# Kernel optimization log

Measured on AMD Instinct MI355X. Metric: run time of the kernel, lower is better.

Reference implementation:

```python
import jax, jax.numpy as jnp
import numpy as np

N = 8192
IN_F = 512
OUT_F = 256
ALPHA = 0.2


def setup_inputs() -> dict:
    key = jax.random.key(0)
    k1, k2, k3 = jax.random.split(key, 3)
    inp = jax.random.normal(k1, (N, IN_F), dtype=jnp.float32)
    # xavier_uniform with gain=1.414
    def xavier(k, shape, gain=1.414):
        fan_in, fan_out = shape[0], shape[1]
        bound = gain * np.sqrt(6.0 / (fan_in + fan_out))
        return jax.random.uniform(k, shape, jnp.float32, -bound, bound)
    W = xavier(k2, (IN_F, OUT_F))
    a = xavier(k3, (2 * OUT_F, 1))
    adj = jnp.ones((N, N), dtype=jnp.int32)  # unused by the original forward
    return {"input": inp, "adj": adj, "W": W, "a": a}


def reference(input, adj, W, a):
    # h: [N, F]
    h = input @ W
    F_ = h.shape[1]
    # Original builds [N, N, 2F] pairwise concat then matmul with a [2F,1].
    # Equivalent: e[i,j] = leaky_relu(h[i] . a[:F] + h[j] . a[F:])
    src = h @ a[:F_, 0]   # [N]
    dst = h @ a[F_:, 0]   # [N]
    e = jax.nn.leaky_relu(src[:, None] + dst[None, :], negative_slope=ALPHA)  # [N, N]
    attention = jax.nn.softmax(e, axis=1)  # adj is NOT applied in original code
    h_prime = attention @ h  # [N, F]
    return jax.nn.elu(h_prime)
```

## Files before the change

### kernel.cpp

```cpp
#include <hip/hip_runtime.h>
#include <math.h>

#define NR 8192
#define INF_ 512
#define OUTF 256
#define ALPHA 0.2f

__global__ __launch_bounds__(256) void k_gemm(const float* __restrict__ A,
                                              const float* __restrict__ W,
                                              float* __restrict__ H) {
    __shared__ float As[16][68];
    __shared__ float Bs[16][68];
    const int tid = threadIdx.x;
    const int brow = blockIdx.x * 64;
    const int bcol = blockIdx.y * 64;
    const int tx = tid & 15, ty = tid >> 4;
    const int ar = tid >> 2;
    const int ac = (tid & 3) << 2;
    const int br = tid >> 4;
    const int bc = (tid & 15) << 2;

    float acc[4][4] = {};
    for (int k0 = 0; k0 < INF_; k0 += 16) {
        float4 av = *(const float4*)(A + (size_t)(brow + ar) * INF_ + k0 + ac);
        float4 bv = *(const float4*)(W + (size_t)(k0 + br) * OUTF + bcol + bc);
        __syncthreads();
        As[ac + 0][ar] = av.x; As[ac + 1][ar] = av.y;
        As[ac + 2][ar] = av.z; As[ac + 3][ar] = av.w;
        *(float4*)&Bs[br][bc] = bv;
        __syncthreads();
#pragma unroll
        for (int kk = 0; kk < 16; ++kk) {
            float4 a4 = *(const float4*)&As[kk][ty * 4];
            float4 b4 = *(const float4*)&Bs[kk][tx * 4];
            acc[0][0] = fmaf(a4.x, b4.x, acc[0][0]); acc[0][1] = fmaf(a4.x, b4.y, acc[0][1]);
            acc[0][2] = fmaf(a4.x, b4.z, acc[0][2]); acc[0][3] = fmaf(a4.x, b4.w, acc[0][3]);
            acc[1][0] = fmaf(a4.y, b4.x, acc[1][0]); acc[1][1] = fmaf(a4.y, b4.y, acc[1][1]);
            acc[1][2] = fmaf(a4.y, b4.z, acc[1][2]); acc[1][3] = fmaf(a4.y, b4.w, acc[1][3]);
            acc[2][0] = fmaf(a4.z, b4.x, acc[2][0]); acc[2][1] = fmaf(a4.z, b4.y, acc[2][1]);
            acc[2][2] = fmaf(a4.z, b4.z, acc[2][2]); acc[2][3] = fmaf(a4.z, b4.w, acc[2][3]);
            acc[3][0] = fmaf(a4.w, b4.x, acc[3][0]); acc[3][1] = fmaf(a4.w, b4.y, acc[3][1]);
            acc[3][2] = fmaf(a4.w, b4.z, acc[3][2]); acc[3][3] = fmaf(a4.w, b4.w, acc[3][3]);
        }
    }
#pragma unroll
    for (int m = 0; m < 4; ++m) {
        float4 o = make_float4(acc[m][0], acc[m][1], acc[m][2], acc[m][3]);
        *(float4*)(H + (size_t)(brow + ty * 4 + m) * OUTF + bcol + tx * 4) = o;
    }
}

__global__ __launch_bounds__(256) void k_srcdst(const float* __restrict__ H,
                                                const float* __restrict__ a,
                                                float* __restrict__ src,
                                                float* __restrict__ dst) {
    const int wv = threadIdx.x >> 6;
    const int ln = threadIdx.x & 63;
    const int row = blockIdx.x * 4 + wv;
    float4 hv = *(const float4*)(H + (size_t)row * OUTF + ln * 4);
    float4 a1 = *(const float4*)(a + ln * 4);
    float4 a2 = *(const float4*)(a + OUTF + ln * 4);
    float s = hv.x * a1.x + hv.y * a1.y + hv.z * a1.z + hv.w * a1.w;
    float d = hv.x * a2.x + hv.y * a2.y + hv.z * a2.z + hv.w * a2.w;
#pragma unroll
    for (int o = 32; o > 0; o >>= 1) {
        s += __shfl_down(s, o);
        d += __shfl_down(d, o);
    }
    if (ln == 0) { src[row] = s; dst[row] = d; }
}

__global__ __launch_bounds__(256) void k_rank(const float* __restrict__ dstv,
                                              float* __restrict__ dsts,
                                              int* __restrict__ perm) {
    __shared__ float key[NR];
    const int tid = threadIdx.x;
#pragma unroll
    for (int i = 0; i < 8; ++i)
        *(float4*)(key + 4 * (tid + 256 * i)) = *(const float4*)(dstv + 4 * (tid + 256 * i));
    __syncthreads();
    const int el = blockIdx.x * 32 + (tid >> 3);
    const int sub = tid & 7;
    const float my = key[el];
    const int sbase = sub << 10;
    int cnt = 0;
#pragma unroll 4
    for (int i = 0; i < 256; ++i) {
        const int off = ((i + sub) << 2) & 1023;
        const int k0 = sbase + off;
        float4 v = *(const float4*)(key + k0);
        cnt += (int)((v.x < my) | ((v.x == my) & (k0 + 0 < el)));
        cnt += (int)((v.y < my) | ((v.y == my) & (k0 + 1 < el)));
        cnt += (int)((v.z < my) | ((v.z == my) & (k0 + 2 < el)));
        cnt += (int)((v.w < my) | ((v.w == my) & (k0 + 3 < el)));
    }
    cnt += __shfl_down(cnt, 4);
    cnt += __shfl_down(cnt, 2);
    cnt += __shfl_down(cnt, 1);
    if (sub == 0) {
        dsts[cnt] = my;
        perm[cnt] = el;
    }
}

__global__ __launch_bounds__(1024) void k_scan(const float* __restrict__ dsts,
                                               float* __restrict__ wplus,
                                               float* __restrict__ wminus,
                                               float* __restrict__ Splus,
                                               float* __restrict__ Sminus) {
    __shared__ float wsP[16], wsM[16];
    const int t = threadIdx.x;
    const int lane = t & 63;
    const float D = dsts[NR - 1];
    float4 v0 = *(const float4*)(dsts + t * 8);
    float4 v1 = *(const float4*)(dsts + t * 8 + 4);
    float vv[8] = {v0.x, v0.y, v0.z, v0.w, v1.x, v1.y, v1.z, v1.w};
    float wp[8], wm[8];
    float sp = 0.f, sm = 0.f;
#pragma unroll
    for (int j = 0; j < 8; ++j) {
        wp[j] = expf(vv[j] - D);
        wm[j] = expf(ALPHA * vv[j]);
        sp += wp[j]; sm += wm[j];
    }
    *(float4*)(wplus + t * 8)      = make_float4(wp[0], wp[1], wp[2], wp[3]);
    *(float4*)(wplus + t * 8 + 4)  = make_float4(wp[4], wp[5], wp[6], wp[7]);
    *(float4*)(wminus + t * 8)     = make_float4(wm[0], wm[1], wm[2], wm[3]);
    *(float4*)(wminus + t * 8 + 4) = make_float4(wm[4], wm[5], wm[6], wm[7]);
    float ip = sp, im = sm;
#pragma unroll
    for (int o = 1; o < 64; o <<= 1) {
        float tp = __shfl_up(ip, o);
        float tm = __shfl_up(im, o);
        if (lane >= o) { ip += tp; im += tm; }
    }
    if (lane == 63) { wsP[t >> 6] = ip; wsM[t >> 6] = im; }
    __syncthreads();
    if (t < 16) {
        float a = wsP[t], b = wsM[t];
#pragma unroll
        for (int o = 1; o < 16; o <<= 1) {
            float ta = __shfl_up(a, o);
            float tb = __shfl_up(b, o);
            if (t >= o) { a += ta; b += tb; }
        }
        wsP[t] = a; wsM[t] = b;
    }
    __syncthreads();
    const int w = t >> 6;
    float rp = (w ? wsP[w - 1] : 0.f) + (ip - sp);
    float rm = (w ? wsM[w - 1] : 0.f) + (im - sm);
#pragma unroll
    for (int j = 0; j < 8; ++j) {
        rp += wp[j]; rm += wm[j];
        Splus[t * 8 + j + 1] = rp;
        Sminus[t * 8 + j + 1] = rm;
    }
    if (t == 0) { Splus[0] = 0.f; Sminus[0] = 0.f; }
}

__global__ __launch_bounds__(256) void k_chunksum(const float* __restrict__ H,
                                                  const int* __restrict__ perm,
                                                  const float* __restrict__ wplus,
                                                  const float* __restrict__ wminus,
                                                  float* __restrict__ chunkP,
                                                  float* __restrict__ chunkM) {
    const int b = blockIdx.x, f = threadIdx.x;
    float aP = 0.f, aM = 0.f;
#pragma unroll 4
    for (int k = 0; k < 32; ++k) {
        int g = b * 32 + k;
        int p = perm[g];
        float hv = H[(size_t)p * OUTF + f];
        aP = fmaf(wplus[g], hv, aP);
        aM = fmaf(wminus[g], hv, aM);
    }
    chunkP[b * OUTF + f] = aP;
    chunkM[b * OUTF + f] = aM;
}

__global__ __launch_bounds__(64) void k_chunkscan(const float* __restrict__ chunkP,
                                                  const float* __restrict__ chunkM,
                                                  float* __restrict__ offP,
                                                  float* __restrict__ offM,
                                                  float* __restrict__ PrefP,
                                                  float* __restrict__ PrefM) {
    const int f = blockIdx.x;
    const bool minus = (blockIdx.y != 0);
    const float* sv = minus ? chunkM : chunkP;
    float* dv = minus ? offM : offP;
    float* tot = minus ? PrefM : PrefP;
    const int l = threadIdx.x;
    float v0 = sv[(4 * l + 0) * OUTF + f];
    float v1 = sv[(4 * l + 1) * OUTF + f];
    float v2 = sv[(4 * l + 2) * OUTF + f];
    float v3 = sv[(4 * l + 3) * OUTF + f];
    float s = v0 + v1 + v2 + v3;
    float incl = s;
#pragma unroll
    for (int o = 1; o < 64; o <<= 1) {
        float t = __shfl_up(incl, o);
        if (l >= o) incl += t;
    }
    float excl = incl - s;
    dv[(4 * l + 0) * OUTF + f] = excl;
    dv[(4 * l + 1) * OUTF + f] = excl + v0;
    dv[(4 * l + 2) * OUTF + f] = excl + v0 + v1;
    dv[(4 * l + 3) * OUTF + f] = excl + v0 + v1 + v2;
    if (l == 63) tot[(size_t)NR * OUTF + f] = incl;
}

__global__ __launch_bounds__(256) void k_writepref(const float* __restrict__ H,
                                                   const int* __restrict__ perm,
                                                   const float* __restrict__ wplus,
                                                   const float* __restrict__ wminus,
                                                   const float* __restrict__ offP,
                                                   const float* __restrict__ offM,
                                                   float* __restrict__ PrefP,
                                                   float* __restrict__ PrefM) {
    const int b = blockIdx.x, f = threadIdx.x;
    float aP = offP[b * OUTF + f];
    float aM = offM[b * OUTF + f];
    for (int k = 0; k < 32; ++k) {
        int g = b * 32 + k;
        PrefP[(size_t)g * OUTF + f] = aP;
        PrefM[(size_t)g * OUTF + f] = aM;
        int p = perm[g];
        float hv = H[(size_t)p * OUTF + f];
        aP = fmaf(wplus[g], hv, aP);
        aM = fmaf(wminus[g], hv, aM);
    }
}

__global__ __launch_bounds__(256) void k_out(const float* __restrict__ src,
                                             const float* __restrict__ dsts,
                                             const float* __restrict__ Splus,
                                             const float* __restrict__ Sminus,
                                             const float* __restrict__ PrefP,
                                             const float* __restrict__ PrefM,
                                             float* __restrict__ out) {
    const int i = blockIdx.x, f = threadIdx.x;
    const float si = src[i];
    const float D = dsts[NR - 1];
    const float thr = -si;
    int lo = 0, hi = NR;
    while (lo < hi) {
        int mid = (lo + hi) >> 1;
        if (dsts[mid] <= thr) lo = mid + 1; else hi = mid;
    }
    const int t = lo;
    const float cP = expf(si + D);
    const float cM = expf(ALPHA * si);
    const float SP = Splus[NR] - Splus[t];
    const float SM = Sminus[t];
    const float inv = 1.f / (cP * SP + cM * SM);
    const float pP = PrefP[(size_t)NR * OUTF + f] - PrefP[(size_t)t * OUTF + f];
    const float pM = PrefM[(size_t)t * OUTF + f];
    const float v = (cP * pP + cM * pM) * inv;
    out[(size_t)i * OUTF + f] = v > 0.f ? v : expm1f(v);
}

extern "C" void kernel_launch(void* const* d_in, const int* in_sizes, int n_in,
                              void* d_out, int out_size, void* d_ws, size_t ws_size,
                              hipStream_t stream) {
    const float* X = (const float*)d_in[0];
    const float* W = (const float*)d_in[2];
    const float* a = (const float*)d_in[3];
    float* out = (float*)d_out;

    char* ws = (char*)d_ws;
    size_t off = 0;
    auto carve = [&](size_t bytes) -> void* {
        void* p = ws + off;
        off += (bytes + 1023) & ~(size_t)1023;
        return p;
    };
    float* H      = (float*)carve((size_t)NR * OUTF * 4);
    float* src    = (float*)carve(NR * 4);
    float* dstv   = (float*)carve(NR * 4);
    float* dsts   = (float*)carve(NR * 4);
    int*   perm   = (int*)carve(NR * 4);
    float* wplus  = (float*)carve(NR * 4);
    float* wminus = (float*)carve(NR * 4);
    float* Splus  = (float*)carve((NR + 1) * 4);
    float* Sminus = (float*)carve((NR + 1) * 4);
    float* chunkP = (float*)carve(256 * OUTF * 4);
    float* chunkM = (float*)carve(256 * OUTF * 4);
    float* offP   = (float*)carve(256 * OUTF * 4);
    float* offM   = (float*)carve(256 * OUTF * 4);
    float* PrefP  = (float*)carve((size_t)(NR + 1) * OUTF * 4);
    float* PrefM  = (float*)carve((size_t)(NR + 1) * OUTF * 4);

    k_gemm<<<dim3(NR / 64, OUTF / 64), 256, 0, stream>>>(X, W, H);
    k_srcdst<<<NR / 4, 256, 0, stream>>>(H, a, src, dstv);
    k_rank<<<NR / 32, 256, 0, stream>>>(dstv, dsts, perm);
    k_scan<<<1, 1024, 0, stream>>>(dsts, wplus, wminus, Splus, Sminus);
    k_chunksum<<<256, 256, 0, stream>>>(H, perm, wplus, wminus, chunkP, chunkM);
    k_chunkscan<<<dim3(OUTF, 2), 64, 0, stream>>>(chunkP, chunkM, offP, offM, PrefP, PrefM);
    k_writepref<<<256, 256, 0, stream>>>(H, perm, wplus, wminus, offP, offM, PrefP, PrefM);
    k_out<<<NR, 256, 0, stream>>>(src, dsts, Splus, Sminus, PrefP, PrefM, out);
}
```

Measured before the change: 444.4 us.

## Use split-bf16 MFMA GEMM and fuse post-GEMM stages into one cooperative kernel

Replaces the FP32 SIMT GEMM with a matrix-core GEMM that splits each operand into hi and lo bf16 parts and uses three MFMAs per tile to keep near-FP32 accuracy. The seven post-GEMM kernels (src/dst, rank sort, scan, chunk sums, chunk scan, prefix write, output) are merged into one 256-block cooperative kernel separated by grid syncs. The scan is parallelised across blocks, and the output stage handles 32 rows per block. This removes launch overhead and uses the matrix cores, at the cost of grid-sync latency, lower parallelism in the final stage, and some precision loss from the bf16 split.

```diff
diff --git a/kernel.cpp b/kernel.cpp
--- a/kernel.cpp
+++ b/kernel.cpp
@@ -1,263 +1,296 @@
 #include <hip/hip_runtime.h>
+#include <hip/hip_cooperative_groups.h>
 #include <math.h>
+
+namespace cg = cooperative_groups;
 
 #define NR 8192
 #define INF_ 512
 #define OUTF 256
 #define ALPHA 0.2f
 
-__global__ __launch_bounds__(256) void k_gemm(const float* __restrict__ A,
+typedef __attribute__((ext_vector_type(8))) short bf16x8;
+typedef __attribute__((ext_vector_type(4))) float f32x4;
+
+#define MFMA(a, b, c) __builtin_amdgcn_mfma_f32_16x16x32_bf16((a), (b), (c), 0, 0, 0)
+
+__device__ __forceinline__ ushort f2bf(float x) {
+    unsigned u = __float_as_uint(x);
+    return (ushort)((u + 0x7fff + ((u >> 16) & 1)) >> 16);
+}
+__device__ __forceinline__ float bf2f(ushort b) { return __uint_as_float((unsigned)b << 16); }
+
+__global__ __launch_bounds__(256) void k_gemm(const float* __restrict__ X,
                                               const float* __restrict__ W,
                                               float* __restrict__ H) {
-    __shared__ float As[16][68];
-    __shared__ float Bs[16][68];
+    __shared__ ushort sAhi[2048], sAlo[2048], sBhi[2048], sBlo[2048];
     const int tid = threadIdx.x;
-    const int brow = blockIdx.x * 64;
-    const int bcol = blockIdx.y * 64;
-    const int tx = tid & 15, ty = tid >> 4;
-    const int ar = tid >> 2;
-    const int ac = (tid & 3) << 2;
-    const int br = tid >> 4;
-    const int bc = (tid & 15) << 2;
-
-    float acc[4][4] = {};
-    for (int k0 = 0; k0 < INF_; k0 += 16) {
-        float4 av = *(const float4*)(A + (size_t)(brow + ar) * INF_ + k0 + ac);
-        float4 bv = *(const float4*)(W + (size_t)(k0 + br) * OUTF + bcol + bc);
-        __syncthreads();
-        As[ac + 0][ar] = av.x; As[ac + 1][ar] = av.y;
-        As[ac + 2][ar] = av.z; As[ac + 3][ar] = av.w;
-        *(float4*)&Bs[br][bc] = bv;
-        __syncthreads();
-#pragma unroll
-        for (int kk = 0; kk < 16; ++kk) {
-            float4 a4 = *(const float4*)&As[kk][ty * 4];
-            float4 b4 = *(const float4*)&Bs[kk][tx * 4];
-            acc[0][0] = fmaf(a4.x, b4.x, acc[0][0]); acc[0][1] = fmaf(a4.x, b4.y, acc[0][1]);
-            acc[0][2] = fmaf(a4.x, b4.z, acc[0][2]); acc[0][3] = fmaf(a4.x, b4.w, acc[0][3]);
-            acc[1][0] = fmaf(a4.y, b4.x, acc[1][0]); acc[1][1] = fmaf(a4.y, b4.y, acc[1][1]);
-            acc[1][2] = fmaf(a4.y, b4.z, acc[1][2]); acc[1][3] = fmaf(a4.y, b4.w, acc[1][3]);
-            acc[2][0] = fmaf(a4.z, b4.x, acc[2][0]); acc[2][1] = fmaf(a4.z, b4.y, acc[2][1]);
-            acc[2][2] = fmaf(a4.z, b4.z, acc[2][2]); acc[2][3] = fmaf(a4.z, b4.w, acc[2][3]);
-            acc[3][0] = fmaf(a4.w, b4.x, acc[3][0]); acc[3][1] = fmaf(a4.w, b4.y, acc[3][1]);
-            acc[3][2] = fmaf(a4.w, b4.z, acc[3][2]); acc[3][3] = fmaf(a4.w, b4.w, acc[3][3]);
-        }
-    }
-#pragma unroll
-    for (int m = 0; m < 4; ++m) {
-        float4 o = make_float4(acc[m][0], acc[m][1], acc[m][2], acc[m][3]);
-        *(float4*)(H + (size_t)(brow + ty * 4 + m) * OUTF + bcol + tx * 4) = o;
+    const int brow = blockIdx.x * 64, bcol = blockIdx.y * 64;
+    const int lane = tid & 63, wr = tid >> 6;
+    const int s_kg = tid >> 6, s_i = tid & 63;
+    const float* gA = X + (size_t)(brow + s_i) * INF_ + s_kg * 8;
+    const float* gB = W + (size_t)(s_kg * 8) * OUTF + bcol + s_i;
+    const int sw = tid * 8;
+    const int fr = lane & 15, kg = lane >> 4;
+    const int aoff = kg * 512 + (wr * 16 + fr) * 8;
+    const int boff = kg * 512 + fr * 8;
+
+    f32x4 acc0 = {0.f,0.f,0.f,0.f}, acc1 = {0.f,0.f,0.f,0.f};
+    f32x4 acc2 = {0.f,0.f,0.f,0.f}, acc3 = {0.f,0.f,0.f,0.f};
+
+    float ra[8], rb[8];
+    {
+        float4 v0 = *(const float4*)gA, v1 = *(const float4*)(gA + 4);
+        ra[0]=v0.x; ra[1]=v0.y; ra[2]=v0.z; ra[3]=v0.w;
+        ra[4]=v1.x; ra[5]=v1.y; ra[6]=v1.z; ra[7]=v1.w;
+#pragma unroll
+        for (int j = 0; j < 8; ++j) rb[j] = gB[j * OUTF];
+    }
+    for (int t = 0; t < INF_ / 32; ++t) {
+        ushort ah[8], al[8], bh[8], bl[8];
+#pragma unroll
+        for (int j = 0; j < 8; ++j) {
+            ah[j] = f2bf(ra[j]); al[j] = f2bf(ra[j] - bf2f(ah[j]));
+            bh[j] = f2bf(rb[j]); bl[j] = f2bf(rb[j] - bf2f(bh[j]));
+        }
+        *(uint4*)&sAhi[sw] = *(uint4*)ah; *(uint4*)&sAlo[sw] = *(uint4*)al;
+        *(uint4*)&sBhi[sw] = *(uint4*)bh; *(uint4*)&sBlo[sw] = *(uint4*)bl;
+        __syncthreads();
+        if (t < INF_ / 32 - 1) {
+            const float* pA = gA + (t + 1) * 32;
+            const float* pB = gB + (size_t)(t + 1) * 32 * OUTF;
+            float4 v0 = *(const float4*)pA, v1 = *(const float4*)(pA + 4);
+            ra[0]=v0.x; ra[1]=v0.y; ra[2]=v0.z; ra[3]=v0.w;
+            ra[4]=v1.x; ra[5]=v1.y; ra[6]=v1.z; ra[7]=v1.w;
+#pragma unroll
+            for (int j = 0; j < 8; ++j) rb[j] = pB[j * OUTF];
+        }
+        bf16x8 ahi = *(const bf16x8*)&sAhi[aoff];
+        bf16x8 alo = *(const bf16x8*)&sAlo[aoff];
+        bf16x8 bh0 = *(const bf16x8*)&sBhi[boff];
+        bf16x8 bl0 = *(const bf16x8*)&sBlo[boff];
+        bf16x8 bh1 = *(const bf16x8*)&sBhi[boff + 128];
+        bf16x8 bl1 = *(const bf16x8*)&sBlo[boff + 128];
+        bf16x8 bh2 = *(const bf16x8*)&sBhi[boff + 256];
+        bf16x8 bl2 = *(const bf16x8*)&sBlo[boff + 256];
+        bf16x8 bh3 = *(const bf16x8*)&sBhi[boff + 384];
+        bf16x8 bl3 = *(const bf16x8*)&sBlo[boff + 384];
+        acc0 = MFMA(ahi, bh0, acc0); acc0 = MFMA(ahi, bl0, acc0); acc0 = MFMA(alo, bh0, acc0);
+        acc1 = MFMA(ahi, bh1, acc1); acc1 = MFMA(ahi, bl1, acc1); acc1 = MFMA(alo, bh1, acc1);
+        acc2 = MFMA(ahi, bh2, acc2); acc2 = MFMA(ahi, bl2, acc2); acc2 = MFMA(alo, bh2, acc2);
+        acc3 = MFMA(ahi, bh3, acc3); acc3 = MFMA(ahi, bl3, acc3); acc3 = MFMA(alo, bh3, acc3);
+        __syncthreads();
+    }
+    const int orow = brow + wr * 16 + kg * 4;
+    const int ocol = bcol + fr;
+#pragma unroll
+    for (int q = 0; q < 4; ++q) {
+        H[(size_t)(orow + q) * OUTF + ocol + 0]  = acc0[q];
+        H[(size_t)(orow + q) * OUTF + ocol + 16] = acc1[q];
+        H[(size_t)(orow + q) * OUTF + ocol + 32] = acc2[q];
+        H[(size_t)(orow + q) * OUTF + ocol + 48] = acc3[q];
     }
 }
 
-__global__ __launch_bounds__(256) void k_srcdst(const float* __restrict__ H,
-                                                const float* __restrict__ a,
-                                                float* __restrict__ src,
-                                                float* __restrict__ dst) {
-    const int wv = threadIdx.x >> 6;
-    const int ln = threadIdx.x & 63;
-    const int row = blockIdx.x * 4 + wv;
-    float4 hv = *(const float4*)(H + (size_t)row * OUTF + ln * 4);
-    float4 a1 = *(const float4*)(a + ln * 4);
-    float4 a2 = *(const float4*)(a + OUTF + ln * 4);
-    float s = hv.x * a1.x + hv.y * a1.y + hv.z * a1.z + hv.w * a1.w;
-    float d = hv.x * a2.x + hv.y * a2.y + hv.z * a2.z + hv.w * a2.w;
-#pragma unroll
-    for (int o = 32; o > 0; o >>= 1) {
-        s += __shfl_down(s, o);
-        d += __shfl_down(d, o);
-    }
-    if (ln == 0) { src[row] = s; dst[row] = d; }
-}
-
-__global__ __launch_bounds__(256) void k_rank(const float* __restrict__ dstv,
-                                              float* __restrict__ dsts,
-                                              int* __restrict__ perm) {
+struct KParams {
+    const float* H; const float* a;
+    float* dstv; float* dsts; int* perm;
+    float* Splus; float* Sminus;
+    float* csP; float* csM; float* ebP; float* ebM;
+    float* chunkP; float* chunkM; float* offP; float* offM;
+    float* PrefP; float* PrefM; float* out;
+};
+
+__global__ __launch_bounds__(256) void k_fused(KParams p) {
+    cg::grid_group grid = cg::this_grid();
     __shared__ float key[NR];
-    const int tid = threadIdx.x;
-#pragma unroll
-    for (int i = 0; i < 8; ++i)
-        *(float4*)(key + 4 * (tid + 256 * i)) = *(const float4*)(dstv + 4 * (tid + 256 * i));
-    __syncthreads();
-    const int el = blockIdx.x * 32 + (tid >> 3);
-    const int sub = tid & 7;
-    const float my = key[el];
-    const int sbase = sub << 10;
-    int cnt = 0;
+    __shared__ float lpP[32], lpM[32];
+    __shared__ float swp[32], swm[32];
+    __shared__ int   sp[32];
+    __shared__ float ws0[4], ws1[4];
+    __shared__ float ssrc[32];
+    __shared__ int   stt[32];
+    __shared__ float scP[32], scM[32], sinv[32];
+
+    const int b = blockIdx.x, tid = threadIdx.x;
+    const int lane = tid & 63, wv = tid >> 6;
+
+    {
+        float4 a1 = *(const float4*)(p.a + lane * 4);
+        float4 a2 = *(const float4*)(p.a + OUTF + lane * 4);
+#pragma unroll
+        for (int j = 0; j < 8; ++j) {
+            int row = b * 32 + wv * 8 + j;
+            float4 hv = *(const float4*)(p.H + (size_t)row * OUTF + lane * 4);
+            float s = hv.x*a1.x + hv.y*a1.y + hv.z*a1.z + hv.w*a1.w;
+            float d = hv.x*a2.x + hv.y*a2.y + hv.z*a2.z + hv.w*a2.w;
+#pragma unroll
+            for (int o = 32; o > 0; o >>= 1) { s += __shfl_down(s, o); d += __shfl_down(d, o); }
+            if (lane == 0) { ssrc[wv * 8 + j] = s; p.dstv[row] = d; }
+        }
+    }
+    __threadfence(); grid.sync();
+
+    {
+#pragma unroll
+        for (int i = 0; i < 8; ++i)
+            *(float4*)(key + 4 * (tid + 256 * i)) = *(const float4*)(p.dstv + 4 * (tid + 256 * i));
+        __syncthreads();
+        const int el = b * 32 + (tid >> 3);
+        const int sub = tid & 7;
+        const float my = key[el];
+        const int sbase = sub << 10;
+        int cnt = 0;
 #pragma unroll 4
-    for (int i = 0; i < 256; ++i) {
-        const int off = ((i + sub) << 2) & 1023;
-        const int k0 = sbase + off;
-        float4 v = *(const float4*)(key + k0);
-        cnt += (int)((v.x < my) | ((v.x == my) & (k0 + 0 < el)));
-        cnt += (int)((v.y < my) | ((v.y == my) & (k0 + 1 < el)));
-        cnt += (int)((v.z < my) | ((v.z == my) & (k0 + 2 < el)));
-        cnt += (int)((v.w < my) | ((v.w == my) & (k0 + 3 < el)));
-    }
-    cnt += __shfl_down(cnt, 4);
-    cnt += __shfl_down(cnt, 2);
-    cnt += __shfl_down(cnt, 1);
-    if (sub == 0) {
-        dsts[cnt] = my;
-        perm[cnt] = el;
-    }
-}
-
-__global__ __launch_bounds__(1024) void k_scan(const float* __restrict__ dsts,
-                                               float* __restrict__ wplus,
-                                               float* __restrict__ wminus,
-                                               float* __restrict__ Splus,
-                                               float* __restrict__ Sminus) {
-    __shared__ float wsP[16], wsM[16];
-    const int t = threadIdx.x;
-    const int lane = t & 63;
-    const float D = dsts[NR - 1];
-    float4 v0 = *(const float4*)(dsts + t * 8);
-    float4 v1 = *(const float4*)(dsts + t * 8 + 4);
-    float vv[8] = {v0.x, v0.y, v0.z, v0.w, v1.x, v1.y, v1.z, v1.w};
-    float wp[8], wm[8];
-    float sp = 0.f, sm = 0.f;
-#pragma unroll
-    for (int j = 0; j < 8; ++j) {
-        wp[j] = expf(vv[j] - D);
-        wm[j] = expf(ALPHA * vv[j]);
-        sp += wp[j]; sm += wm[j];
-    }
-    *(float4*)(wplus + t * 8)      = make_float4(wp[0], wp[1], wp[2], wp[3]);
-    *(float4*)(wplus + t * 8 + 4)  = make_float4(wp[4], wp[5], wp[6], wp[7]);
-    *(float4*)(wminus + t * 8)     = make_float4(wm[0], wm[1], wm[2], wm[3]);
-    *(float4*)(wminus + t * 8 + 4) = make_float4(wm[4], wm[5], wm[6], wm[7]);
-    float ip = sp, im = sm;
-#pragma unroll
-    for (int o = 1; o < 64; o <<= 1) {
-        float tp = __shfl_up(ip, o);
-        float tm = __shfl_up(im, o);
-        if (lane >= o) { ip += tp; im += tm; }
-    }
-    if (lane == 63) { wsP[t >> 6] = ip; wsM[t >> 6] = im; }
-    __syncthreads();
-    if (t < 16) {
-        float a = wsP[t], b = wsM[t];
-#pragma unroll
-        for (int o = 1; o < 16; o <<= 1) {
-            float ta = __shfl_up(a, o);
-            float tb = __shfl_up(b, o);
-            if (t >= o) { a += ta; b += tb; }
-        }
-        wsP[t] = a; wsM[t] = b;
-    }
-    __syncthreads();
-    const int w = t >> 6;
-    float rp = (w ? wsP[w - 1] : 0.f) + (ip - sp);
-    float rm = (w ? wsM[w - 1] : 0.f) + (im - sm);
-#pragma unroll
-    for (int j = 0; j < 8; ++j) {
-        rp += wp[j]; rm += wm[j];
-        Splus[t * 8 + j + 1] = rp;
-        Sminus[t * 8 + j + 1] = rm;
-    }
-    if (t == 0) { Splus[0] = 0.f; Sminus[0] = 0.f; }
-}
-
-__global__ __launch_bounds__(256) void k_chunksum(const float* __restrict__ H,
-                                                  const int* __restrict__ perm,
-                                                  const float* __restrict__ wplus,
-                                                  const float* __restrict__ wminus,
-                                                  float* __restrict__ chunkP,
-                                                  float* __restrict__ chunkM) {
-    const int b = blockIdx.x, f = threadIdx.x;
-    float aP = 0.f, aM = 0.f;
-#pragma unroll 4
-    for (int k = 0; k < 32; ++k) {
-        int g = b * 32 + k;
-        int p = perm[g];
-        float hv = H[(size_t)p * OUTF + f];
-        aP = fmaf(wplus[g], hv, aP);
-        aM = fmaf(wminus[g], hv, aM);
-    }
-    chunkP[b * OUTF + f] = aP;
-    chunkM[b * OUTF + f] = aM;
-}
-
-__global__ __launch_bounds__(64) void k_chunkscan(const float* __restrict__ chunkP,
-                                                  const float* __restrict__ chunkM,
-                                                  float* __restrict__ offP,
-                                                  float* __restrict__ offM,
-                                                  float* __restrict__ PrefP,
-                                                  float* __restrict__ PrefM) {
-    const int f = blockIdx.x;
-    const bool minus = (blockIdx.y != 0);
-    const float* sv = minus ? chunkM : chunkP;
-    float* dv = minus ? offM : offP;
-    float* tot = minus ? PrefM : PrefP;
-    const int l = threadIdx.x;
-    float v0 = sv[(4 * l + 0) * OUTF + f];
-    float v1 = sv[(4 * l + 1) * OUTF + f];
-    float v2 = sv[(4 * l + 2) * OUTF + f];
-    float v3 = sv[(4 * l + 3) * OUTF + f];
-    float s = v0 + v1 + v2 + v3;
-    float incl = s;
-#pragma unroll
-    for (int o = 1; o < 64; o <<= 1) {
-        float t = __shfl_up(incl, o);
-        if (l >= o) incl += t;
-    }
-    float excl = incl - s;
-    dv[(4 * l + 0) * OUTF + f] = excl;
-    dv[(4 * l + 1) * OUTF + f] = excl + v0;
-    dv[(4 * l + 2) * OUTF + f] = excl + v0 + v1;
-    dv[(4 * l + 3) * OUTF + f] = excl + v0 + v1 + v2;
-    if (l == 63) tot[(size_t)NR * OUTF + f] = incl;
-}
-
-__global__ __launch_bounds__(256) void k_writepref(const float* __restrict__ H,
-                                                   const int* __restrict__ perm,
-                                                   const float* __restrict__ wplus,
-                                                   const float* __restrict__ wminus,
-                                                   const float* __restrict__ offP,
-                                                   const float* __restrict__ offM,
-                                                   float* __restrict__ PrefP,
-                                                   float* __restrict__ PrefM) {
-    const int b = blockIdx.x, f = threadIdx.x;
-    float aP = offP[b * OUTF + f];
-    float aM = offM[b * OUTF + f];
-    for (int k = 0; k < 32; ++k) {
-        int g = b * 32 + k;
-        PrefP[(size_t)g * OUTF + f] = aP;
-        PrefM[(size_t)g * OUTF + f] = aM;
-        int p = perm[g];
-        float hv = H[(size_t)p * OUTF + f];
-        aP = fmaf(wplus[g], hv, aP);
-        aM = fmaf(wminus[g], hv, aM);
-    }
-}
-
-__global__ __launch_bounds__(256) void k_out(const float* __restrict__ src,
-                                             const float* __restrict__ dsts,
-                                             const float* __restrict__ Splus,
-                                             const float* __restrict__ Sminus,
-                                             const float* __restrict__ PrefP,
-                                             const float* __restrict__ PrefM,
-                                             float* __restrict__ out) {
-    const int i = blockIdx.x, f = threadIdx.x;
-    const float si = src[i];
-    const float D = dsts[NR - 1];
-    const float thr = -si;
-    int lo = 0, hi = NR;
-    while (lo < hi) {
-        int mid = (lo + hi) >> 1;
-        if (dsts[mid] <= thr) lo = mid + 1; else hi = mid;
-    }
-    const int t = lo;
-    const float cP = expf(si + D);
-    const float cM = expf(ALPHA * si);
-    const float SP = Splus[NR] - Splus[t];
-    const float SM = Sminus[t];
-    const float inv = 1.f / (cP * SP + cM * SM);
-    const float pP = PrefP[(size_t)NR * OUTF + f] - PrefP[(size_t)t * OUTF + f];
-    const float pM = PrefM[(size_t)t * OUTF + f];
-    const float v = (cP * pP + cM * pM) * inv;
-    out[(size_t)i * OUTF + f] = v > 0.f ? v : expm1f(v);
+        for (int i = 0; i < 256; ++i) {
+            const int off = ((i + sub) << 2) & 1023;
+            const int k0 = sbase + off;
+            float4 v = *(const float4*)(key + k0);
+            cnt += (int)((v.x < my) | ((v.x == my) & (k0 + 0 < el)));
+            cnt += (int)((v.y < my) | ((v.y == my) & (k0 + 1 < el)));
+            cnt += (int)((v.z < my) | ((v.z == my) & (k0 + 2 < el)));
+            cnt += (int)((v.w < my) | ((v.w == my) & (k0 + 3 < el)));
+        }
+        cnt += __shfl_down(cnt, 4);
+        cnt += __shfl_down(cnt, 2);
+        cnt += __shfl_down(cnt, 1);
+        if (sub == 0) { p.dsts[cnt] = my; p.perm[cnt] = el; }
+    }
+    __threadfence(); grid.sync();
+
+    const float D = p.dsts[NR - 1];
+
+    if (tid < 32) {
+        int g = b * 32 + tid;
+        float kv = p.dsts[g];
+        float wp = expf(kv - D), wm = expf(ALPHA * kv);
+        swp[tid] = wp; swm[tid] = wm;
+        sp[tid] = p.perm[g];
+        float ip = wp, im = wm;
+#pragma unroll
+        for (int o = 1; o < 32; o <<= 1) {
+            float tp = __shfl_up(ip, o), tm = __shfl_up(im, o);
+            if (tid >= o) { ip += tp; im += tm; }
+        }
+        lpP[tid] = ip; lpM[tid] = im;
+        if (tid == 31) { p.csP[b] = ip; p.csM[b] = im; }
+    }
+    __threadfence(); grid.sync();
+
+    if (b == 0) {
+        float vP = p.csP[tid], vM = p.csM[tid];
+        float iP = vP, iM = vM;
+#pragma unroll
+        for (int o = 1; o < 64; o <<= 1) {
+            float tP = __shfl_up(iP, o), tM = __shfl_up(iM, o);
+            if (lane >= o) { iP += tP; iM += tM; }
+        }
+        if (lane == 63) { ws0[wv] = iP; ws1[wv] = iM; }
+        __syncthreads();
+        float bP = 0.f, bM = 0.f;
+#pragma unroll
+        for (int w = 0; w < 4; ++w) if (w < wv) { bP += ws0[w]; bM += ws1[w]; }
+        p.ebP[tid] = bP + iP - vP;
+        p.ebM[tid] = bM + iM - vM;
+    }
+    __threadfence(); grid.sync();
+
+    if (tid < 32) {
+        int g = b * 32 + tid;
+        float bP = p.ebP[b], bM = p.ebM[b];
+        p.Splus[g + 1]  = bP + lpP[tid];
+        p.Sminus[g + 1] = bM + lpM[tid];
+    }
+    if (b == 0 && tid == 0) { p.Splus[0] = 0.f; p.Sminus[0] = 0.f; }
+
+    {
+        const int f = tid;
+        float aP = 0.f, aM = 0.f;
+        for (int k0 = 0; k0 < 32; k0 += 8) {
+            float hv[8];
+#pragma unroll
+            for (int j = 0; j < 8; ++j) hv[j] = p.H[(size_t)sp[k0 + j] * OUTF + f];
+#pragma unroll
+            for (int j = 0; j < 8; ++j) {
+                aP = fmaf(swp[k0 + j], hv[j], aP);
+                aM = fmaf(swm[k0 + j], hv[j], aM);
+            }
+        }
+        p.chunkP[(size_t)b * OUTF + f] = aP;
+        p.chunkM[(size_t)b * OUTF + f] = aM;
+    }
+    __threadfence(); grid.sync();
+
+    {
+        const int fc = b;
+        float vP = p.chunkP[(size_t)tid * OUTF + fc];
+        float vM = p.chunkM[(size_t)tid * OUTF + fc];
+        float iP = vP, iM = vM;
+#pragma unroll
+        for (int o = 1; o < 64; o <<= 1) {
+            float tP = __shfl_up(iP, o), tM = __shfl_up(iM, o);
+            if (lane >= o) { iP += tP; iM += tM; }
+        }
+        if (lane == 63) { ws0[wv] = iP; ws1[wv] = iM; }
+        __syncthreads();
+        float bP = 0.f, bM = 0.f;
+#pragma unroll
+        for (int w = 0; w < 4; ++w) if (w < wv) { bP += ws0[w]; bM += ws1[w]; }
+        iP += bP; iM += bM;
+        p.offP[(size_t)tid * OUTF + fc] = iP - vP;
+        p.offM[(size_t)tid * OUTF + fc] = iM - vM;
+        if (tid == 255) {
+            p.PrefP[(size_t)NR * OUTF + fc] = iP;
+            p.PrefM[(size_t)NR * OUTF + fc] = iM;
+        }
+    }
+    __threadfence(); grid.sync();
+
+    {
+        const int f = tid;
+        float aP = p.offP[(size_t)b * OUTF + f];
+        float aM = p.offM[(size_t)b * OUTF + f];
+        for (int k0 = 0; k0 < 32; k0 += 8) {
+            float hv[8];
+#pragma unroll
+            for (int j = 0; j < 8; ++j) hv[j] = p.H[(size_t)sp[k0 + j] * OUTF + f];
+#pragma unroll
+            for (int j = 0; j < 8; ++j) {
+                int g = b * 32 + k0 + j;
+                p.PrefP[(size_t)g * OUTF + f] = aP;
+                p.PrefM[(size_t)g * OUTF + f] = aM;
+                aP = fmaf(swp[k0 + j], hv[j], aP);
+                aM = fmaf(swm[k0 + j], hv[j], aM);
+            }
+        }
+    }
+    __threadfence(); grid.sync();
+
+    {
+        const float SPtot = p.Splus[NR];
+        if (tid < 32) {
+            float si = ssrc[tid];
+            float thr = -si;
+            int lo = 0, hi = NR;
+            while (lo < hi) {
+                int mid = (lo + hi) >> 1;
+                if (p.dsts[mid] <= thr) lo = mid + 1; else hi = mid;
+            }
+            float cP = expf(si + D), cM = expf(ALPHA * si);
+            float SP = SPtot - p.Splus[lo], SM = p.Sminus[lo];
+            stt[tid] = lo; scP[tid] = cP; scM[tid] = cM;
+            sinv[tid] = 1.f / (cP * SP + cM * SM);
+        }
+        __syncthreads();
+        const float totP = p.PrefP[(size_t)NR * OUTF + tid];
+        for (int r = 0; r < 32; ++r) {
+            int t_ = stt[r];
+            float pPv = totP - p.PrefP[(size_t)t_ * OUTF + tid];
+            float pMv = p.PrefM[(size_t)t_ * OUTF + tid];
+            float v = (scP[r] * pPv + scM[r] * pMv) * sinv[r];
+            p.out[(size_t)(b * 32 + r) * OUTF + tid] = v > 0.f ? v : expm1f(v);
+        }
+    }
 }
 
 extern "C" void kernel_launch(void* const* d_in, const int* in_sizes, int n_in,
@@ -271,19 +304,20 @@
     char* ws = (char*)d_ws;
     size_t off = 0;
     auto carve = [&](size_t bytes) -> void* {
-        void* p = ws + off;
+        void* ptr = ws + off;
         off += (bytes + 1023) & ~(size_t)1023;
-        return p;
+        return ptr;
     };
     float* H      = (float*)carve((size_t)NR * OUTF * 4);
-    float* src    = (float*)carve(NR * 4);
     float* dstv   = (float*)carve(NR * 4);
     float* dsts   = (float*)carve(NR * 4);
     int*   perm   = (int*)carve(NR * 4);
-    float* wplus  = (float*)carve(NR * 4);
-    float* wminus = (float*)carve(NR * 4);
     float* Splus  = (float*)carve((NR + 1) * 4);
     float* Sminus = (float*)carve((NR + 1) * 4);
+    float* csP    = (float*)carve(256 * 4);
+    float* csM    = (float*)carve(256 * 4);
+    float* ebP    = (float*)carve(256 * 4);
+    float* ebM    = (float*)carve(256 * 4);
     float* chunkP = (float*)carve(256 * OUTF * 4);
     float* chunkM = (float*)carve(256 * OUTF * 4);
     float* offP   = (float*)carve(256 * OUTF * 4);
@@ -292,11 +326,14 @@
     float* PrefM  = (float*)carve((size_t)(NR + 1) * OUTF * 4);
 
     k_gemm<<<dim3(NR / 64, OUTF / 64), 256, 0, stream>>>(X, W, H);
-    k_srcdst<<<NR / 4, 256, 0, stream>>>(H, a, src, dstv);
-    k_rank<<<NR / 32, 256, 0, stream>>>(dstv, dsts, perm);
-    k_scan<<<1, 1024, 0, stream>>>(dsts, wplus, wminus, Splus, Sminus);
-    k_chunksum<<<256, 256, 0, stream>>>(H, perm, wplus, wminus, chunkP, chunkM);
-    k_chunkscan<<<dim3(OUTF, 2), 64, 0, stream>>>(chunkP, chunkM, offP, offM, PrefP, PrefM);
-    k_writepref<<<256, 256, 0, stream>>>(H, perm, wplus, wminus, offP, offM, PrefP, PrefM);
-    k_out<<<NR, 256, 0, stream>>>(src, dsts, Splus, Sminus, PrefP, PrefM, out);
+
+    KParams p;
+    p.H = H; p.a = a; p.dstv = dstv; p.dsts = dsts; p.perm = perm;
+    p.Splus = Splus; p.Sminus = Sminus;
+    p.csP = csP; p.csM = csM; p.ebP = ebP; p.ebM = ebM;
+    p.chunkP = chunkP; p.chunkM = chunkM; p.offP = offP; p.offM = offM;
+    p.PrefP = PrefP; p.PrefM = PrefM; p.out = out;
+    void* args[] = {&p};
+    hipLaunchCooperativeKernel((const void*)k_fused, dim3(256), dim3(256),
+                               args, 0, stream);
 }
```

New measurement: 786.7 us. +77.0%, slower.
